# Kernel optimization log

Measured on AMD Instinct MI355X. Metric: run time of the kernel, lower is better.

Reference implementation:

```python
import math
import jax, jax.numpy as jnp
import numpy as np
from jax.scipy.special import erf, erfinv, logsumexp

M = 250000          # number of (u, v) datapoints
P = 4               # n_phases
N_MC = 64           # MC samples per interface pair
IA, IB = np.triu_indices(P, 1)   # interface pair indices (Ia < Ib since I is increasing)
K = len(IA)                      # n_interfaces = 6
LOG2 = math.log(2.0)
LOG2PI = math.log(2.0 * math.pi)
LOG_GAMMA_3_2 = math.log(math.gamma(1.5))


def _logsinh(x):
    # numerically stable log(sinh(x)); x > 0 in all uses here
    s = jnp.abs(x)
    return -LOG2 + s + jnp.log1p(-jnp.exp(-2.0 * s))


def _log_bessel_05(x):
    # I_{1/2}(x) = sqrt(2/(pi x)) sinh(x)
    return 0.5 * LOG2 - 0.5 * jnp.log(math.pi * x) + _logsinh(x)


def setup_inputs() -> dict:
    key = jax.random.key(0)
    k0, k1, k2 = jax.random.split(key, 3)
    u = jax.random.uniform(k0, (M,), dtype=jnp.float32)                 # intensities in [0,1]
    v = jax.random.uniform(k1, (M,), dtype=jnp.float32) * 0.3 + 0.01    # gradient magnitudes > 0
    eps = jax.random.uniform(k2, (K, N_MC), dtype=jnp.float32)          # fresh MC draw per interface
    I = jnp.linspace(0.0, 1.0, P, dtype=jnp.float32)
    W = jnp.zeros((K + P,), dtype=jnp.float32)
    sigma_b = jnp.array([2.0], dtype=jnp.float32)
    sigma_n = jnp.array([0.1], dtype=jnp.float32)
    d = jnp.array([2.0], dtype=jnp.float32)
    r = jnp.array([0.05], dtype=jnp.float32)
    return {"u": u, "v": v, "eps": eps, "I": I, "W": W,
            "sigma_b": sigma_b, "sigma_n": sigma_n, "d": d, "r": r}


def reference(u, v, eps, I, W, sigma_b, sigma_n, d, r):
    sb = sigma_b[0]
    sn = sigma_n[0]
    dd = d[0]
    rho = jnp.tanh(r[0])
    sr = sn * jnp.sqrt(1.0 - rho)          # sigma_n * sqrt(1 - rho)
    s2 = sn ** 2 * (1.0 - rho)
    N = eps.shape[1]
    log_w = jax.nn.log_softmax(W)

    # interior phases: [P, M]
    interior = (LOG2 + 2.0 * jnp.log(v) - LOG_GAMMA_3_2 - 3.0 * jnp.log(sr)
                - (v / sr) ** 2 - jnp.log(sn) - 0.5 * LOG2PI
                - 0.5 * ((u - I[:, None]) / sn) ** 2)

    rows = [interior]
    log_v = jnp.log(v)
    v2 = v ** 2
    for k in range(K):  # small fixed loop over interface pairs
        Ia = I[IA[k]]
        Ib = I[IB[k]]
        x = eps[k] * 2.0 * dd * sb - dd * sb                              # [N]
        In = (erf(x / (math.sqrt(2.0) * sb)) + 1.0) * 0.5 * (Ib - Ia) + Ia  # [N]
        # log p(u | I): [N, M]
        lu = -jnp.log(sn) - 0.5 * LOG2PI - 0.5 * ((u[None, :] - In[:, None]) / sn) ** 2
        # G(I): [N]
        Gk = (Ib - Ia) / jnp.sqrt(2.0 * math.pi * sb ** 2) * jnp.exp(
            -erfinv(2.0 * (In - Ia) / (Ib - Ia) - 1.0) ** 2)
        # log p(v | I): [N, M]
        lb = _log_bessel_05(2.0 * v[None, :] * Gk[:, None] / s2)
        lv = (LOG2 - 2.0 * jnp.log(sr) + 1.5 * log_v[None, :]
              - 0.5 * jnp.log(Gk)[:, None] + lb
              - (v2[None, :] + Gk[:, None] ** 2) / s2)
        rows.append((-math.log(N) + logsumexp(lu + lv, axis=0))[None, :])

    log_p = jnp.concatenate(rows, axis=0)                 # [P + K, M]
    log_p_uv = logsumexp(log_w[:, None] + log_p, axis=0)  # [M]
    return -jnp.sum(log_p_uv) / u.shape[0]
```

## Files before the change

### kernel.cpp

```cpp
#include <hip/hip_runtime.h>
#include <math.h>

#define KN 384
#define TPB 256

__device__ double g_part[1024];
__device__ int    g_ctr = 0;

__device__ __forceinline__ float fexp2(float x) {
  return __builtin_amdgcn_exp2f(x);
}

__global__ __launch_bounds__(TPB, 4) void fused_kernel(
    const float* __restrict__ u, const float* __restrict__ v,
    const float* __restrict__ eps, const float* __restrict__ I,
    const float* __restrict__ W, const float* __restrict__ sb_,
    const float* __restrict__ sn_, const float* __restrict__ d_,
    const float* __restrict__ r_, float* __restrict__ out,
    int M, int nb) {
  __shared__ float stx[KN], sty[KN], stz[KN];
  __shared__ double red[TPB];
  __shared__ int    slast;
  const int tid = threadIdx.x;
  const int i   = blockIdx.x * TPB + tid;

  float uu = 0.f, vv = 1.f;
  if (i < M) { uu = u[i]; vv = v[i]; }

  const float sb  = sb_[0];
  const float sn  = sn_[0];
  const float dd  = d_[0];
  const float rho = tanhf(r_[0]);
  const float s2  = sn * sn * (1.f - rho);
  const float sr  = sqrtf(s2);
  const float isn = 1.f / sn;
  const float inv_s2 = 1.f / s2;
  const float LOG2E = 1.4426950408889634f;
  const float SQH   = sqrtf(0.5f * LOG2E);

  float wmax = W[0];
  for (int j = 1; j < 10; ++j) wmax = fmaxf(wmax, W[j]);
  float se = 0.f;
  for (int j = 0; j < 10; ++j) se += expf(W[j] - wmax);
  const float lse = wmax + logf(se);

  const float LOG2PI_ = 1.8378770664093453f;
  const float LOG2_   = 0.6931471805599453f;
  const float LGG32   = -0.12078223763524522f;
  const float LOGPI_  = 1.1447298858494002f;
  const float Cterm = -logf(sn) - 0.5f * LOG2PI_ - logf(sr) - 0.5f * LOGPI_;
  const float Cint0 = LOG2_ - LGG32 - 3.f * logf(sr) - logf(sn) - 0.5f * LOG2PI_;

  float wint[4], cq[4];
#pragma unroll
  for (int p = 0; p < 4; ++p) {
    wint[p] = expf(W[p] - lse + Cint0);
    cq[p]   = I[p] * isn * SQH;
  }

  const int IAc[6] = {0, 0, 0, 1, 1, 2};
  const int IBc[6] = {1, 2, 3, 2, 3, 3};
  for (int t = tid; t < KN; t += TPB) {
    const int k = t >> 6;
    const float Ia = I[IAc[k]], Ib = I[IBc[k]];
    const float wk = expf(W[4 + k] - lse + Cterm) * (1.0f / 64.0f);
    const float e  = eps[t];
    const float x  = e * 2.f * dd * sb - dd * sb;
    const float y  = x / (1.4142135623730951f * sb);
    const float In = (erff(y) + 1.f) * 0.5f * (Ib - Ia) + Ia;
    const float qq = 2.f * (In - Ia) / (Ib - Ia) - 1.f;
    const float gi = erfinvf(qq);
    const float G  = (Ib - Ia) * 0.3989422804014327f / sb * expf(-gi * gi);
    stx[t] = In * isn * SQH;
    sty[t] = 2.f * inv_s2 * G * LOG2E;
    stz[t] = wk * expf(-G * G * inv_s2) / G;
  }

  const float us = uu * isn * SQH;
  const float gg = fexp2(-vv * vv * inv_s2 * LOG2E);
  float aint = 0.f;
#pragma unroll
  for (int p = 0; p < 4; ++p) {
    const float dq = us - cq[p];
    aint = fmaf(wint[p], fexp2(-dq * dq), aint);
  }
  const float c0 = (i < M) ? vv * gg : 0.f;
  const float c1 = (i < M) ? vv * vv * gg * aint : 1.f;

  __syncthreads();

  float S0 = 0.f, S1 = 0.f, S2 = 0.f, S3 = 0.f;
#pragma unroll 2
  for (int t = 0; t < KN; t += 4) {
    const float4 X = *(const float4*)(stx + t);
    const float4 Y = *(const float4*)(sty + t);
    const float4 Z = *(const float4*)(stz + t);
    {
      const float du = us - X.x, nd = du * -du;
      const float a1 = fmaf(vv, Y.x, nd), a2 = fmaf(vv, -Y.x, nd);
      S0 = fmaf(Z.x, fexp2(a1), S0);
      S0 = fmaf(-Z.x, fexp2(a2), S0);
    }
    {
      const float du = us - X.y, nd = du * -du;
      const float a1 = fmaf(vv, Y.y, nd), a2 = fmaf(vv, -Y.y, nd);
      S1 = fmaf(Z.y, fexp2(a1), S1);
      S1 = fmaf(-Z.y, fexp2(a2), S1);
    }
    {
      const float du = us - X.z, nd = du * -du;
      const float a1 = fmaf(vv, Y.z, nd), a2 = fmaf(vv, -Y.z, nd);
      S2 = fmaf(Z.z, fexp2(a1), S2);
      S2 = fmaf(-Z.z, fexp2(a2), S2);
    }
    {
      const float du = us - X.w, nd = du * -du;
      const float a1 = fmaf(vv, Y.w, nd), a2 = fmaf(vv, -Y.w, nd);
      S3 = fmaf(Z.w, fexp2(a1), S3);
      S3 = fmaf(-Z.w, fexp2(a2), S3);
    }
  }
  const float S = (S0 + S1) + (S2 + S3);

  double mysum = (double)__logf(fmaf(c0, S, c1));

  red[tid] = mysum;
  __syncthreads();
  for (int s = TPB / 2; s > 0; s >>= 1) {
    if (tid < s) red[tid] += red[tid + s];
    __syncthreads();
  }
  if (tid == 0)
    __hip_atomic_store(&g_part[blockIdx.x], red[0], __ATOMIC_RELAXED,
                       __HIP_MEMORY_SCOPE_AGENT);

  if (tid == 0) {
    const int c = __hip_atomic_fetch_add(&g_ctr, 1, __ATOMIC_ACQ_REL,
                                         __HIP_MEMORY_SCOPE_AGENT);
    slast = (c == nb - 1) ? 1 : 0;
  }
  __syncthreads();
  if (slast) {
    double s = 0.0;
    for (int j = tid; j < nb; j += TPB)
      s += __hip_atomic_load(&g_part[j], __ATOMIC_RELAXED,
                             __HIP_MEMORY_SCOPE_AGENT);
    red[tid] = s;
    __syncthreads();
    for (int k2 = TPB / 2; k2 > 0; k2 >>= 1) {
      if (tid < k2) red[tid] += red[tid + k2];
      __syncthreads();
    }
    if (tid == 0) {
      out[0] = (float)(-red[0] / (double)M);
      __hip_atomic_store(&g_ctr, 0, __ATOMIC_RELAXED,
                         __HIP_MEMORY_SCOPE_AGENT);
    }
  }
}

extern "C" void kernel_launch(void* const* d_in, const int* in_sizes, int n_in,
                              void* d_out, int out_size, void* d_ws, size_t ws_size,
                              hipStream_t stream) {
  const float* u   = (const float*)d_in[0];
  const float* v   = (const float*)d_in[1];
  const float* eps = (const float*)d_in[2];
  const float* I   = (const float*)d_in[3];
  const float* W   = (const float*)d_in[4];
  const float* sb  = (const float*)d_in[5];
  const float* sn  = (const float*)d_in[6];
  const float* dd  = (const float*)d_in[7];
  const float* r   = (const float*)d_in[8];
  const int M  = in_sizes[0];
  const int nb = (M + TPB - 1) / TPB;
  hipLaunchKernelGGL(fused_kernel, dim3(nb), dim3(TPB), 0, stream,
                     u, v, eps, I, W, sb, sn, dd, r, (float*)d_out, M, nb);
}
```

Measured before the change: 106.6 us.

## Split MC sum across two threads per point and use packed float2 math

New measurement: 111.8 us. 4.8% more time.

```diff
diff --git a/kernel.cpp b/kernel.cpp
--- a/kernel.cpp
+++ b/kernel.cpp
@@ -3,8 +3,11 @@
 
 #define KN 384
 #define TPB 256
+#define PPB 128
 
-__device__ double g_part[1024];
+typedef float v2f __attribute__((ext_vector_type(2)));
+
+__device__ double g_part[2048];
 __device__ int    g_ctr = 0;
 
 __device__ __forceinline__ float fexp2(float x) {
@@ -18,11 +21,14 @@
     const float* __restrict__ sn_, const float* __restrict__ d_,
     const float* __restrict__ r_, float* __restrict__ out,
     int M, int nb) {
-  __shared__ float stx[KN], sty[KN], stz[KN];
+  __shared__ __align__(16) float stx[KN], sty[KN], stz[KN];
+  __shared__ float  sS[PPB];
   __shared__ double red[TPB];
   __shared__ int    slast;
   const int tid = threadIdx.x;
-  const int i   = blockIdx.x * TPB + tid;
+  const int pi  = tid & (PPB - 1);
+  const int h   = tid >> 7;
+  const int i   = blockIdx.x * PPB + pi;
 
   float uu = 0.f, vv = 1.f;
   if (i < M) { uu = u[i]; vv = v[i]; }
@@ -89,40 +95,51 @@
 
   __syncthreads();
 
-  float S0 = 0.f, S1 = 0.f, S2 = 0.f, S3 = 0.f;
-#pragma unroll 2
-  for (int t = 0; t < KN; t += 4) {
-    const float4 X = *(const float4*)(stx + t);
-    const float4 Y = *(const float4*)(sty + t);
-    const float4 Z = *(const float4*)(stz + t);
+  const v2f us2 = {us, us};
+  const v2f vv2 = {vv, vv};
+  v2f SPa = {0.f, 0.f}, SMa = {0.f, 0.f};
+  v2f SPb = {0.f, 0.f}, SMb = {0.f, 0.f};
+  const float4* px = (const float4*)(stx + h * (KN / 2));
+  const float4* py = (const float4*)(sty + h * (KN / 2));
+  const float4* pz = (const float4*)(stz + h * (KN / 2));
+#pragma unroll 4
+  for (int j = 0; j < KN / 8; ++j) {
+    const float4 X = px[j], Y = py[j], Z = pz[j];
     {
-      const float du = us - X.x, nd = du * -du;
-      const float a1 = fmaf(vv, Y.x, nd), a2 = fmaf(vv, -Y.x, nd);
-      S0 = fmaf(Z.x, fexp2(a1), S0);
-      S0 = fmaf(-Z.x, fexp2(a2), S0);
+      const v2f tx2 = {X.x, X.y}, ty2 = {Y.x, Y.y}, tz2 = {Z.x, Z.y};
+      const v2f du = us2 - tx2;
+      const v2f nd = du * -du;
+      const v2f a1 = __builtin_elementwise_fma(vv2,  ty2, nd);
+      const v2f a2 = __builtin_elementwise_fma(vv2, -ty2, nd);
+      v2f e1, e2;
+      e1.x = fexp2(a1.x); e1.y = fexp2(a1.y);
+      e2.x = fexp2(a2.x); e2.y = fexp2(a2.y);
+      SPa = __builtin_elementwise_fma(tz2, e1, SPa);
+      SMa = __builtin_elementwise_fma(tz2, e2, SMa);
     }
     {
-      const float du = us - X.y, nd = du * -du;
-      const float a1 = fmaf(vv, Y.y, nd), a2 = fmaf(vv, -Y.y, nd);
-      S1 = fmaf(Z.y, fexp2(a1), S1);
-      S1 = fmaf(-Z.y, fexp2(a2), S1);
-    }
-    {
-      const float du = us - X.z, nd = du * -du;
-      const float a1 = fmaf(vv, Y.z, nd), a2 = fmaf(vv, -Y.z, nd);
-      S2 = fmaf(Z.z, fexp2(a1), S2);
-      S2 = fmaf(-Z.z, fexp2(a2), S2);
-    }
-    {
-      const float du = us - X.w, nd = du * -du;
-      const float a1 = fmaf(vv, Y.w, nd), a2 = fmaf(vv, -Y.w, nd);
-      S3 = fmaf(Z.w, fexp2(a1), S3);
-      S3 = fmaf(-Z.w, fexp2(a2), S3);
+      const v2f tx2 = {X.z, X.w}, ty2 = {Y.z, Y.w}, tz2 = {Z.z, Z.w};
+      const v2f du = us2 - tx2;
+      const v2f nd = du * -du;
+      const v2f a1 = __builtin_elementwise_fma(vv2,  ty2, nd);
+      const v2f a2 = __builtin_elementwise_fma(vv2, -ty2, nd);
+      v2f e1, e2;
+      e1.x = fexp2(a1.x); e1.y = fexp2(a1.y);
+      e2.x = fexp2(a2.x); e2.y = fexp2(a2.y);
+      SPb = __builtin_elementwise_fma(tz2, e1, SPb);
+      SMb = __builtin_elementwise_fma(tz2, e2, SMb);
     }
   }
-  const float S = (S0 + S1) + (S2 + S3);
+  const float Shalf = ((SPa.x + SPa.y) + (SPb.x + SPb.y))
+                    - ((SMa.x + SMa.y) + (SMb.x + SMb.y));
 
-  double mysum = (double)__logf(fmaf(c0, S, c1));
+  if (h == 0) sS[pi] = Shalf;
+  __syncthreads();
+  double mysum = 0.0;
+  if (h == 1) {
+    const float S = sS[pi] + Shalf;
+    mysum = (double)__logf(fmaf(c0, S, c1));
+  }
 
   red[tid] = mysum;
   __syncthreads();
@@ -172,7 +189,7 @@
   const float* dd  = (const float*)d_in[7];
   const float* r   = (const float*)d_in[8];
   const int M  = in_sizes[0];
-  const int nb = (M + TPB - 1) / TPB;
+  const int nb = (M + PPB - 1) / PPB;
   hipLaunchKernelGGL(fused_kernel, dim3(nb), dim3(TPB), 0, stream,
                      u, v, eps, I, W, sb, sn, dd, r, (float*)d_out, M, nb);
 }
```
